# Optimization experiments

Hardware: AMD Instinct MI355X
Metric: run time of the kernel (lower is better)

## Reference

```python
import jax, jax.numpy as jnp
import numpy as np

VOXEL_SIZE = 96
SHARPNESS = 100.0
EPS = 1e-8


def _grid_coords(V):
    # matches torch: x fastest, normalized by (V-1); shape [V*V, 2] as (x, y)
    y, x = jnp.meshgrid(jnp.arange(V, dtype=jnp.float32), jnp.arange(V, dtype=jnp.float32), indexing='ij')
    return jnp.stack([x.ravel(), y.ravel()], axis=1) / float(V - 1)


def setup_inputs() -> dict:
    key = jax.random.key(0)
    k1, k2, k3 = jax.random.split(key, 3)
    B, N, P = 4, 32, 32
    polygons = jax.random.uniform(k1, (B, N, P, 2), dtype=jnp.float32)
    attributes = jax.random.uniform(k2, (B, 8), dtype=jnp.float32)
    validity_scores = jax.random.uniform(k3, (B, N), dtype=jnp.float32)
    return {"polygons": polygons, "attributes": attributes, "validity_scores": validity_scores}


def _polygon_masks(polygons, coords):
    # polygons: [B,N,P,2], coords: [M,2] -> soft occupancy masks [B,N,M]
    v0 = polygons                              # [B,N,P,2]
    v1 = jnp.roll(polygons, -1, axis=2)        # next vertex (closed loop)
    e = v1 - v0                                # edges [B,N,P,2]
    pts = coords[None, None, None]             # [1,1,1,M,2]
    v = pts - v0[:, :, :, None, :]             # [B,N,P,M,2]
    e_sq = (e * e).sum(-1) + EPS               # [B,N,P]
    t = (v * e[:, :, :, None, :]).sum(-1) / e_sq[..., None]   # [B,N,P,M]
    t = jnp.clip(t, 0.0, 1.0)
    proj = v0[:, :, :, None, :] + t[..., None] * e[:, :, :, None, :]
    diff = pts - proj
    dists = jnp.sqrt((diff * diff).sum(-1))    # [B,N,P,M]
    min_dist = dists.min(axis=2)               # [B,N,M] min over edges
    # ray-casting point-in-polygon (horizontal ray toward +x)
    x_pts = coords[:, 0]                        # [M]
    y_pts = coords[:, 1]
    x0, y0 = v0[..., 0:1], v0[..., 1:2]        # [B,N,P,1]
    x1, y1 = v1[..., 0:1], v1[..., 1:2]
    y_crosses = ((y0 <= y_pts) & (y1 > y_pts)) | ((y1 <= y_pts) & (y0 > y_pts))
    inter_x = x0 + (x1 - x0) * ((y_pts - y0) / (y1 - y0 + EPS))
    crossings = (inter_x > x_pts) & y_crosses  # [B,N,P,M]
    inside = (crossings.sum(axis=2) % 2) == 1  # [B,N,M]
    sdf = jnp.where(inside, -min_dist, min_dist)
    return jax.nn.sigmoid(-sdf * SHARPNESS)    # [B,N,M]


def reference(polygons, attributes, validity_scores):
    B = polygons.shape[0]
    V = VOXEL_SIZE
    coords = _grid_coords(V)                                   # [V*V, 2]
    masks = _polygon_masks(polygons, coords)                   # [B,N,M]
    valid = validity_scores >= 0.5                             # [B,N]
    combined = jnp.max(jnp.where(valid[:, :, None], masks, 0.0), axis=1)  # [B,M]
    combined = combined.reshape(B, V, V)                       # [B,H,W]
    # height extrusion: int(round(clamp(attr,0,1)*D)), clamped to [1,D]; non-differentiable
    norm_h = jnp.clip(attributes[:, 0], 0.0, 1.0)
    hv = jnp.clip(jnp.round(norm_h * V), 1.0, float(V))        # [B]
    hv = jax.lax.stop_gradient(hv)
    depth_mask = (jnp.arange(V, dtype=jnp.float32)[None, :] < hv[:, None]).astype(combined.dtype)  # [B,D]
    voxels = combined[:, None, :, :] * depth_mask[:, :, None, None]  # [B,D,H,W]
    return voxels
```

## Files before the change

kernel.cpp:

```cpp
#include <hip/hip_runtime.h>

#define V 96
#define VV (V * V)
#define V3 (V * V * V)
#define B_ 4
#define N_ 32
#define P_ 32
#define NE (N_ * P_)
#define TILE 64
#define TPB 256
#define SPLITS 4
#define TILES_PER_B (VV / TILE)

__global__ __launch_bounds__(TPB) void fused_kernel(
    const float* __restrict__ poly,
    const float* __restrict__ attr,
    const float* __restrict__ validity,
    float4* __restrict__ out)
{
    __shared__ float4 se0[NE];
    __shared__ float4 se1[NE];
    __shared__ float2 sraw[NE];
    __shared__ float  spart[SPLITS][TILE];
    __shared__ __align__(16) float sfinal[TILE];
    __shared__ int svalidIdx[N_];
    __shared__ int scnt;

    const int b       = blockIdx.x / TILES_PER_B;
    const int tileInB = blockIdx.x - b * TILES_PER_B;
    const int pix0    = tileInB * TILE;
    const int tid     = threadIdx.x;
    const int s       = tid >> 6;
    const int lane    = tid & 63;

    {
        const float4* pg = (const float4*)(poly + (size_t)b * (N_ * P_ * 2));
        float4 q0 = pg[2 * tid];
        float4 q1 = pg[2 * tid + 1];
        float4* sr4 = (float4*)sraw;
        sr4[2 * tid]     = q0;
        sr4[2 * tid + 1] = q1;
    }
    if (tid < 64) {
        bool v = (tid < N_) && (validity[b * N_ + tid] >= 0.5f);
        unsigned long long m = __ballot(v);
        if (v) {
            int pos = __popcll(m & ((1ull << tid) - 1));
            svalidIdx[pos] = tid;
        }
        if (tid == 0) scnt = (int)__popcll(m);
    }
    __syncthreads();

    #pragma unroll
    for (int i = 0; i < 4; ++i) {
        int e  = 4 * tid + i;
        int p  = e & (P_ - 1);
        int nb = e & ~(P_ - 1);
        int en = nb | ((p + 1) & (P_ - 1));
        float2 v0 = sraw[e];
        float2 v1 = sraw[en];
        float ex = v1.x - v0.x, ey = v1.y - v0.y;
        se0[e] = make_float4(v0.x, v0.y, ex, ey);
        se1[e] = make_float4(__builtin_amdgcn_rcpf(ex * ex + ey * ey + 1e-8f),
                             __builtin_amdgcn_rcpf(ey + 1e-8f),
                             v1.y,
                             0.0f);
    }
    __syncthreads();

    const int pixel = pix0 + lane;
    const int py_i  = pixel / V;
    const int px_i  = pixel - py_i * V;
    const float px = (float)px_i / 95.0f;
    const float py = (float)py_i / 95.0f;

    const int cnt = scnt;
    float pmax = 0.0f;

    for (int j = s; j < cnt; j += SPLITS) {
        const int base = svalidIdx[j] << 5;
        float mind2 = 1e30f;
        int par = 0;
        #pragma unroll
        for (int p = 0; p < P_; ++p) {
            float4 e0 = se0[base + p];
            float4 e1 = se1[base + p];
            float vx = px - e0.x, vy = py - e0.y;
            float t  = (vx * e0.z + vy * e0.w) * e1.x;
            t = fminf(fmaxf(t, 0.0f), 1.0f);
            float dx = vx - t * e0.z, dy = vy - t * e0.w;
            float d2 = dx * dx + dy * dy;
            mind2 = fminf(mind2, d2);
            bool c0 = (e0.y <= py);
            bool c1 = (e1.z <= py);
            float inter_x = e0.x + e0.z * ((py - e0.y) * e1.y);
            par ^= (int)((c0 != c1) & (inter_x > px));
        }
        float mind = sqrtf(mind2);
        float sdf  = par ? -mind : mind;
        float m = 1.0f / (1.0f + __expf(sdf * 100.0f));
        pmax = fmaxf(pmax, m);
    }

    spart[s][lane] = pmax;
    __syncthreads();
    float f = fmaxf(fmaxf(spart[0][lane], spart[1][lane]),
                    fmaxf(spart[2][lane], spart[3][lane]));
    if (s == 0) sfinal[lane] = f;
    __syncthreads();

    float a  = attr[b * 8];
    float nh = fminf(fmaxf(a, 0.0f), 1.0f);
    float hv = fminf(fmaxf(rintf(nh * (float)V), 1.0f), (float)V);
    int hvi = (int)hv;

    const float4* sf4 = (const float4*)sfinal;
    const float4 val = sf4[lane & 15];
    size_t obase = (size_t)b * (V3 / 4) + (size_t)(pix0 >> 2) + (lane & 15);
    #pragma unroll
    for (int k = 0; k < 6; ++k) {
        int d = s * 24 + k * 4 + (lane >> 4);
        float keep = (d < hvi) ? 1.0f : 0.0f;
        out[obase + (size_t)d * (VV / 4)] =
            make_float4(val.x * keep, val.y * keep, val.z * keep, val.w * keep);
    }
}

extern "C" void kernel_launch(void* const* d_in, const int* in_sizes, int n_in,
                              void* d_out, int out_size, void* d_ws, size_t ws_size,
                              hipStream_t stream) {
    const float* polygons = (const float*)d_in[0];
    const float* attrs    = (const float*)d_in[1];
    const float* validity = (const float*)d_in[2];
    float4* out = (float4*)d_out;

    fused_kernel<<<B_ * TILES_PER_B, TPB, 0, stream>>>(polygons, attrs, validity, out);
}
```

Measured before the change: 76.17 us.

## Broadcast polygon edge data via readlane instead of shared memory tables

Removes the shared-memory staging of edge data and the extra barrier. Each lane now loads one vertex pair from global memory per polygon and computes that edge's derived values, and the inner loop broadcasts them to the whole wave with v_readlane into scalar registers. This replaces per-iteration LDS float4 loads with scalar operands. In exchange, every wave recomputes the edge setup for each polygon, and each polygon iteration issues global loads, which rely on L1/L2 hits.

```diff
diff --git a/kernel.cpp b/kernel.cpp
--- a/kernel.cpp
+++ b/kernel.cpp
@@ -6,11 +6,14 @@
 #define B_ 4
 #define N_ 32
 #define P_ 32
-#define NE (N_ * P_)
 #define TILE 64
 #define TPB 256
 #define SPLITS 4
 #define TILES_PER_B (VV / TILE)
+
+__device__ __forceinline__ float rl(float x, int l) {
+    return __uint_as_float(__builtin_amdgcn_readlane(__float_as_uint(x), l));
+}
 
 __global__ __launch_bounds__(TPB) void fused_kernel(
     const float* __restrict__ poly,
@@ -18,10 +21,7 @@
     const float* __restrict__ validity,
     float4* __restrict__ out)
 {
-    __shared__ float4 se0[NE];
-    __shared__ float4 se1[NE];
-    __shared__ float2 sraw[NE];
-    __shared__ float  spart[SPLITS][TILE];
+    __shared__ float spart[SPLITS][TILE];
     __shared__ __align__(16) float sfinal[TILE];
     __shared__ int svalidIdx[N_];
     __shared__ int scnt;
@@ -33,14 +33,6 @@
     const int s       = tid >> 6;
     const int lane    = tid & 63;
 
-    {
-        const float4* pg = (const float4*)(poly + (size_t)b * (N_ * P_ * 2));
-        float4 q0 = pg[2 * tid];
-        float4 q1 = pg[2 * tid + 1];
-        float4* sr4 = (float4*)sraw;
-        sr4[2 * tid]     = q0;
-        sr4[2 * tid + 1] = q1;
-    }
     if (tid < 64) {
         bool v = (tid < N_) && (validity[b * N_ + tid] >= 0.5f);
         unsigned long long m = __ballot(v);
@@ -52,23 +44,6 @@
     }
     __syncthreads();
 
-    #pragma unroll
-    for (int i = 0; i < 4; ++i) {
-        int e  = 4 * tid + i;
-        int p  = e & (P_ - 1);
-        int nb = e & ~(P_ - 1);
-        int en = nb | ((p + 1) & (P_ - 1));
-        float2 v0 = sraw[e];
-        float2 v1 = sraw[en];
-        float ex = v1.x - v0.x, ey = v1.y - v0.y;
-        se0[e] = make_float4(v0.x, v0.y, ex, ey);
-        se1[e] = make_float4(__builtin_amdgcn_rcpf(ex * ex + ey * ey + 1e-8f),
-                             __builtin_amdgcn_rcpf(ey + 1e-8f),
-                             v1.y,
-                             0.0f);
-    }
-    __syncthreads();
-
     const int pixel = pix0 + lane;
     const int py_i  = pixel / V;
     const int px_i  = pixel - py_i * V;
@@ -76,25 +51,42 @@
     const float py = (float)py_i / 95.0f;
 
     const int cnt = scnt;
+    const int p_  = lane & (P_ - 1);
+    const float2* f2base = (const float2*)poly + (size_t)b * (N_ * P_);
+
     float pmax = 0.0f;
 
     for (int j = s; j < cnt; j += SPLITS) {
-        const int base = svalidIdx[j] << 5;
+        const int nidx = svalidIdx[j];
+        const float2* f2 = f2base + nidx * P_;
+        float2 v0 = f2[p_];
+        float2 v1 = f2[(p_ + 1) & (P_ - 1)];
+        float aex = v1.x - v0.x;
+        float aey = v1.y - v0.y;
+        float arq = __builtin_amdgcn_rcpf(aex * aex + aey * aey + 1e-8f);
+        float ary = __builtin_amdgcn_rcpf(aey + 1e-8f);
+        float ax0 = v0.x, ay0 = v0.y, ay1 = v1.y;
+
         float mind2 = 1e30f;
         int par = 0;
         #pragma unroll
         for (int p = 0; p < P_; ++p) {
-            float4 e0 = se0[base + p];
-            float4 e1 = se1[base + p];
-            float vx = px - e0.x, vy = py - e0.y;
-            float t  = (vx * e0.z + vy * e0.w) * e1.x;
+            float x0 = rl(ax0, p);
+            float y0 = rl(ay0, p);
+            float ex = rl(aex, p);
+            float ey = rl(aey, p);
+            float rq = rl(arq, p);
+            float ry = rl(ary, p);
+            float y1 = rl(ay1, p);
+            float vx = px - x0, vy = py - y0;
+            float t  = (vx * ex + vy * ey) * rq;
             t = fminf(fmaxf(t, 0.0f), 1.0f);
-            float dx = vx - t * e0.z, dy = vy - t * e0.w;
+            float dx = vx - t * ex, dy = vy - t * ey;
             float d2 = dx * dx + dy * dy;
             mind2 = fminf(mind2, d2);
-            bool c0 = (e0.y <= py);
-            bool c1 = (e1.z <= py);
-            float inter_x = e0.x + e0.z * ((py - e0.y) * e1.y);
+            bool c0 = (y0 <= py);
+            bool c1 = (y1 <= py);
+            float inter_x = x0 + ex * (vy * ry);
             par ^= (int)((c0 != c1) & (inter_x > px));
         }
         float mind = sqrtf(mind2);
```

New measurement: 80.06 us. 5.1% more time.
